# Kernel optimization log

Measured on AMD Instinct MI355X. Metric: run time of the kernel, lower is better.

The kernel has to match this reference:

```python
import jax, jax.numpy as jnp
import numpy as np

NUM_EXPERTS = 8
TOP_K = 2
HIDDEN = 2048
INTER = 7168
B, S = 4, 2048


def setup_inputs() -> dict:
    key = jax.random.key(0)
    k0, k1, k2, k3, k4 = jax.random.split(key, 5)
    scale_h = 1.0 / np.sqrt(HIDDEN)
    scale_i = 1.0 / np.sqrt(INTER)
    return {
        "hidden_states": jax.random.normal(k0, (B, S, HIDDEN), dtype=jnp.float32),
        "gate_w": jax.random.normal(k1, (NUM_EXPERTS, HIDDEN), dtype=jnp.float32) * scale_h,
        "w1": jax.random.normal(k2, (NUM_EXPERTS, INTER, HIDDEN), dtype=jnp.float32) * scale_h,
        "w3": jax.random.normal(k3, (NUM_EXPERTS, INTER, HIDDEN), dtype=jnp.float32) * scale_h,
        "w2": jax.random.normal(k4, (NUM_EXPERTS, HIDDEN, INTER), dtype=jnp.float32) * scale_i,
    }


def reference(hidden_states, gate_w, w1, w3, w2):
    orig_shape = hidden_states.shape
    x = hidden_states.reshape(-1, HIDDEN)              # [T, H]

    # Router: gate linear -> softmax -> top-k -> renormalize.
    router_logits = x @ gate_w.T                       # [T, E]
    probs = jax.nn.softmax(router_logits, axis=-1)
    topk_w, topk_idx = jax.lax.top_k(probs, TOP_K)     # [T, K]
    topk_w = topk_w / jnp.sum(topk_w, axis=-1, keepdims=True)

    # Dense combine weights: [T, E] with top-k renormalized weights scattered.
    combine = jnp.sum(
        jax.nn.one_hot(topk_idx, NUM_EXPERTS, dtype=x.dtype) * topk_w[..., None],
        axis=1,
    )                                                   # [T, E]

    out = jnp.zeros_like(x)
    # Fixed small loop over experts (structurally distinct weight matrices);
    # avoids materializing a [T, E, I] intermediate.
    for e in range(NUM_EXPERTS):
        g = jax.nn.silu(x @ w1[e].T)                   # [T, I]
        u = x @ w3[e].T                                # [T, I]
        y = (g * u) @ w2[e].T                          # [T, H]
        out = out + combine[:, e:e + 1] * y

    return out.reshape(orig_shape)
```

## Files before the change

### kernel.cpp

```cpp
#include <hip/hip_runtime.h>
#include <stdint.h>

#define NE    8
#define HID   2048
#define INTER 7168
#define TTOK  8192

typedef __bf16 bf16;
typedef bf16 bf16x4 __attribute__((ext_vector_type(4)));
typedef bf16 bf16x8 __attribute__((ext_vector_type(8)));
typedef float f32x4 __attribute__((ext_vector_type(4)));

__device__ __forceinline__ void glds16(const void* g, void* l) {
  __builtin_amdgcn_global_load_lds((__attribute__((address_space(1))) void*)g,
                                   (__attribute__((address_space(3))) void*)l, 16, 0, 0);
}

__global__ void cvt_f32_bf16(const float* __restrict__ src, bf16* __restrict__ dst, long n) {
  long i = (long)blockIdx.x * blockDim.x + threadIdx.x;
  long stride = (long)gridDim.x * blockDim.x;
  for (long j = i * 4; j < n; j += stride * 4) {
    float4 v = *(const float4*)(src + j);
    bf16x4 o = {(bf16)v.x, (bf16)v.y, (bf16)v.z, (bf16)v.w};
    *(bf16x4*)(dst + j) = o;
  }
}

__global__ void router_kernel(const float* __restrict__ x, const float* __restrict__ gw,
                              int* __restrict__ topk_e, float* __restrict__ topk_w) {
  const int wid = threadIdx.x >> 6, lane = threadIdx.x & 63;
  const int t = blockIdx.x * 4 + wid;
  if (t >= TTOK) return;
  const float* xr = x + (size_t)t * HID;
  float xv[32];
#pragma unroll
  for (int i = 0; i < 32; ++i) xv[i] = xr[lane + 64 * i];
  float lg[NE];
#pragma unroll
  for (int e = 0; e < NE; ++e) {
    const float* g = gw + e * HID;
    float s = 0.f;
#pragma unroll
    for (int i = 0; i < 32; ++i) s += xv[i] * g[lane + 64 * i];
#pragma unroll
    for (int off = 32; off; off >>= 1) s += __shfl_down(s, off);
    lg[e] = s;
  }
  if (lane == 0) {
    int i1 = 0;
#pragma unroll
    for (int e = 1; e < NE; ++e) if (lg[e] > lg[i1]) i1 = e;
    int i2 = (i1 == 0) ? 1 : 0;
#pragma unroll
    for (int e = 0; e < NE; ++e) if (e != i2 && e != i1 && lg[e] > lg[i2]) i2 = e;
    float r = __expf(lg[i2] - lg[i1]);
    float wa = 1.f / (1.f + r);
    topk_e[2 * t] = i1; topk_e[2 * t + 1] = i2;
    topk_w[2 * t] = wa; topk_w[2 * t + 1] = 1.f - wa;
  }
}

__global__ void gather_kernel(const int* __restrict__ topk_e, const float* __restrict__ topk_w,
                              int* __restrict__ cnt, int* __restrict__ ltok, float* __restrict__ lw) {
  const int t = blockIdx.x * blockDim.x + threadIdx.x;
  if (t >= TTOK) return;
#pragma unroll
  for (int j = 0; j < 2; ++j) {
    int e = topk_e[2 * t + j];
    int s = atomicAdd(&cnt[e], 1);
    ltok[e * TTOK + s] = t;
    lw[e * TTOK + s] = topk_w[2 * t + j];
  }
}

__global__ void prefix_kernel(const int* __restrict__ cnt, int* __restrict__ base) {
  if (threadIdx.x == 0 && blockIdx.x == 0) {
    int b = 0;
    for (int e = 0; e < NE; ++e) { base[e] = b; b += cnt[e]; }
  }
}

__launch_bounds__(256, 2)
__global__ void pass1_kernel(const bf16* __restrict__ xb, const bf16* __restrict__ w1b,
                             const bf16* __restrict__ w3b, bf16* __restrict__ hbuf,
                             const int* __restrict__ cnt, const int* __restrict__ base,
                             const int* __restrict__ ltok) {
  const int e = blockIdx.z;
  const int c = cnt[e];
  const int tm = blockIdx.y;
  if (tm * 128 >= c) return;
  const int tn = blockIdx.x;
  __shared__ __align__(16) bf16 lA[128 * 32];
  __shared__ __align__(16) bf16 lB1[128 * 32];
  __shared__ __align__(16) bf16 lB3[128 * 32];
  const int tid = threadIdx.x;
  const int r0 = tid >> 2, r1 = r0 + 64;
  const int sub = (tid & 3) * 16;
  int s0 = tm * 128 + r0; if (s0 >= c) s0 = c - 1;
  int s1 = tm * 128 + r1; if (s1 >= c) s1 = c - 1;
  const char* gA0 = (const char*)(xb + (size_t)ltok[e * TTOK + s0] * HID) + sub;
  const char* gA1 = (const char*)(xb + (size_t)ltok[e * TTOK + s1] * HID) + sub;
  const char* gB1r0 = (const char*)(w1b + ((size_t)e * INTER + tn * 128 + r0) * HID) + sub;
  const char* gB1r1 = (const char*)(w1b + ((size_t)e * INTER + tn * 128 + r1) * HID) + sub;
  const char* gB3r0 = (const char*)(w3b + ((size_t)e * INTER + tn * 128 + r0) * HID) + sub;
  const char* gB3r1 = (const char*)(w3b + ((size_t)e * INTER + tn * 128 + r1) * HID) + sub;
  bf16* lA0 = &lA[tid * 8];  bf16* lA1 = &lA[(tid + 256) * 8];
  bf16* lB1p0 = &lB1[tid * 8]; bf16* lB1p1 = &lB1[(tid + 256) * 8];
  bf16* lB3p0 = &lB3[tid * 8]; bf16* lB3p1 = &lB3[(tid + 256) * 8];

  const int lane = tid & 63;
  const int wid = tid >> 6;
  const int wm = wid >> 1, wn = wid & 1;
  const int ln15 = lane & 15, kq = lane >> 4;

  f32x4 ag[4][4], au[4][4];
#pragma unroll
  for (int m = 0; m < 4; ++m)
#pragma unroll
    for (int n = 0; n < 4; ++n) {
      ag[m][n] = (f32x4){0.f, 0.f, 0.f, 0.f};
      au[m][n] = (f32x4){0.f, 0.f, 0.f, 0.f};
    }

  for (int kt = 0; kt < HID / 32; ++kt) {
    const int kb = kt * 64;
    __syncthreads();
    glds16(gA0 + kb, lA0);   glds16(gA1 + kb, lA1);
    glds16(gB1r0 + kb, lB1p0); glds16(gB1r1 + kb, lB1p1);
    glds16(gB3r0 + kb, lB3p0); glds16(gB3r1 + kb, lB3p1);
    __syncthreads();
    bf16x8 af[4];
#pragma unroll
    for (int m = 0; m < 4; ++m)
      af[m] = *(const bf16x8*)&lA[(wm * 64 + m * 16 + ln15) * 32 + kq * 8];
#pragma unroll
    for (int n = 0; n < 4; ++n) {
      bf16x8 b1 = *(const bf16x8*)&lB1[(wn * 64 + n * 16 + ln15) * 32 + kq * 8];
      bf16x8 b3 = *(const bf16x8*)&lB3[(wn * 64 + n * 16 + ln15) * 32 + kq * 8];
#pragma unroll
      for (int m = 0; m < 4; ++m) {
        ag[m][n] = __builtin_amdgcn_mfma_f32_16x16x32_bf16(af[m], b1, ag[m][n], 0, 0, 0);
        au[m][n] = __builtin_amdgcn_mfma_f32_16x16x32_bf16(af[m], b3, au[m][n], 0, 0, 0);
      }
    }
  }

  const int be = base[e];
#pragma unroll
  for (int m = 0; m < 4; ++m) {
#pragma unroll
    for (int j = 0; j < 4; ++j) {
      const int slot = tm * 128 + wm * 64 + m * 16 + kq * 4 + j;
      if (slot < c) {
        bf16* hrow = hbuf + (size_t)(be + slot) * INTER + tn * 128;
#pragma unroll
        for (int n = 0; n < 4; ++n) {
          const int col = wn * 64 + n * 16 + ln15;
          const float g = ag[m][n][j];
          const float u = au[m][n][j];
          const float hv = g / (1.f + __expf(-g)) * u;
          hrow[col] = (bf16)hv;
        }
      }
    }
  }
}

__launch_bounds__(256, 2)
__global__ void pass2_kernel(const bf16* __restrict__ hbuf, const bf16* __restrict__ w2b,
                             float* __restrict__ out, const int* __restrict__ cnt,
                             const int* __restrict__ base, const int* __restrict__ ltok,
                             const float* __restrict__ lw) {
  const int e = blockIdx.z;
  const int c = cnt[e];
  const int tm = blockIdx.y;
  if (tm * 128 >= c) return;
  const int tn = blockIdx.x;
  __shared__ __align__(16) bf16 lA[128 * 32];
  __shared__ __align__(16) bf16 lB[128 * 32];
  const int tid = threadIdx.x;
  const int r0 = tid >> 2, r1 = r0 + 64;
  const int sub = (tid & 3) * 16;
  const int be = base[e];
  int s0 = tm * 128 + r0; if (s0 >= c) s0 = c - 1;
  int s1 = tm * 128 + r1; if (s1 >= c) s1 = c - 1;
  const char* gA0 = (const char*)(hbuf + (size_t)(be + s0) * INTER) + sub;
  const char* gA1 = (const char*)(hbuf + (size_t)(be + s1) * INTER) + sub;
  const char* gB0 = (const char*)(w2b + ((size_t)e * HID + tn * 128 + r0) * INTER) + sub;
  const char* gB1 = (const char*)(w2b + ((size_t)e * HID + tn * 128 + r1) * INTER) + sub;
  bf16* lA0 = &lA[tid * 8]; bf16* lA1 = &lA[(tid + 256) * 8];
  bf16* lB0 = &lB[tid * 8]; bf16* lB1p = &lB[(tid + 256) * 8];

  const int lane = tid & 63;
  const int wid = tid >> 6;
  const int wm = wid >> 1, wn = wid & 1;
  const int ln15 = lane & 15, kq = lane >> 4;

  f32x4 acc[4][4];
#pragma unroll
  for (int m = 0; m < 4; ++m)
#pragma unroll
    for (int n = 0; n < 4; ++n) acc[m][n] = (f32x4){0.f, 0.f, 0.f, 0.f};

  for (int kt = 0; kt < INTER / 32; ++kt) {
    const int kb = kt * 64;
    __syncthreads();
    glds16(gA0 + kb, lA0); glds16(gA1 + kb, lA1);
    glds16(gB0 + kb, lB0); glds16(gB1 + kb, lB1p);
    __syncthreads();
    bf16x8 af[4];
#pragma unroll
    for (int m = 0; m < 4; ++m)
      af[m] = *(const bf16x8*)&lA[(wm * 64 + m * 16 + ln15) * 32 + kq * 8];
#pragma unroll
    for (int n = 0; n < 4; ++n) {
      bf16x8 bf_ = *(const bf16x8*)&lB[(wn * 64 + n * 16 + ln15) * 32 + kq * 8];
#pragma unroll
      for (int m = 0; m < 4; ++m)
        acc[m][n] = __builtin_amdgcn_mfma_f32_16x16x32_bf16(af[m], bf_, acc[m][n], 0, 0, 0);
    }
  }

#pragma unroll
  for (int m = 0; m < 4; ++m) {
#pragma unroll
    for (int j = 0; j < 4; ++j) {
      const int slot = tm * 128 + wm * 64 + m * 16 + kq * 4 + j;
      if (slot < c) {
        const int t = ltok[e * TTOK + slot];
        const float wt = lw[e * TTOK + slot];
        float* orow = out + (size_t)t * HID + tn * 128;
#pragma unroll
        for (int n = 0; n < 4; ++n) {
          const int col = wn * 64 + n * 16 + ln15;
          atomicAdd(orow + col, wt * acc[m][n][j]);
        }
      }
    }
  }
}

extern "C" void kernel_launch(void* const* d_in, const int* in_sizes, int n_in,
                              void* d_out, int out_size, void* d_ws, size_t ws_size,
                              hipStream_t stream) {
  const float* x  = (const float*)d_in[0];
  const float* gw = (const float*)d_in[1];
  const float* w1 = (const float*)d_in[2];
  const float* w3 = (const float*)d_in[3];
  const float* w2 = (const float*)d_in[4];
  float* out = (float*)d_out;

  char* ws = (char*)d_ws;
  size_t off = 0;
  auto take = [&](size_t bytes) -> char* {
    char* p = ws + off;
    off += (bytes + 255) & ~(size_t)255;
    return p;
  };
  bf16* xb    = (bf16*)take((size_t)TTOK * HID * 2);
  bf16* w1b   = (bf16*)take((size_t)NE * INTER * HID * 2);
  bf16* w3b   = (bf16*)take((size_t)NE * INTER * HID * 2);
  bf16* w2b   = (bf16*)take((size_t)NE * HID * INTER * 2);
  bf16* hbuf  = (bf16*)take((size_t)TTOK * 2 * INTER * 2);
  int*   topk_e = (int*)take(TTOK * 2 * 4);
  float* topk_w = (float*)take(TTOK * 2 * 4);
  int*   ltok   = (int*)take(NE * TTOK * 4);
  float* lwgt   = (float*)take(NE * TTOK * 4);
  int*   cntp   = (int*)take(64);
  int*   basep  = (int*)take(64);
  if (off > ws_size) return;

  hipMemsetAsync(d_out, 0, (size_t)out_size * 4, stream);
  hipMemsetAsync(cntp, 0, 64, stream);

  cvt_f32_bf16<<<2048, 256, 0, stream>>>(x,  xb,  (long)TTOK * HID);
  cvt_f32_bf16<<<4096, 256, 0, stream>>>(w1, w1b, (long)NE * INTER * HID);
  cvt_f32_bf16<<<4096, 256, 0, stream>>>(w3, w3b, (long)NE * INTER * HID);
  cvt_f32_bf16<<<4096, 256, 0, stream>>>(w2, w2b, (long)NE * HID * INTER);

  router_kernel<<<TTOK / 4, 256, 0, stream>>>(x, gw, topk_e, topk_w);
  gather_kernel<<<TTOK / 256, 256, 0, stream>>>(topk_e, topk_w, cntp, ltok, lwgt);
  prefix_kernel<<<1, 64, 0, stream>>>(cntp, basep);

  pass1_kernel<<<dim3(INTER / 128, TTOK / 128, NE), 256, 0, stream>>>(
      xb, w1b, w3b, hbuf, cntp, basep, ltok);
  pass2_kernel<<<dim3(HID / 128, TTOK / 128, NE), 256, 0, stream>>>(
      hbuf, w2b, out, cntp, basep, ltok, lwgt);
}
```

Before: 2.324 ms.

## Rewrite expert GEMMs with 256x256 tiles, double-buffered LDS pipeline and swizzle

Both expert GEMM passes now use 512-thread blocks with 256-row token tiles and double-buffered 64-wide K stages. Global-to-LDS loads for later stages are interleaved with four MFMA phases using explicit waitcnt, barriers and setprio. LDS rows are XOR-swizzled to avoid bank conflicts. Pass1 stacks interleaved w1/w3 rows into one B tile by assuming w3b follows w1b contiguously in the workspace. The larger tiles raise data reuse and hide load latency, but increase LDS and register pressure and reduce the number of blocks.

```diff
diff --git a/kernel.cpp b/kernel.cpp
--- a/kernel.cpp
+++ b/kernel.cpp
@@ -5,6 +5,8 @@
 #define HID   2048
 #define INTER 7168
 #define TTOK  8192
+#define NT1   (HID / 64)
+#define NT2   (INTER / 64)
 
 typedef __bf16 bf16;
 typedef bf16 bf16x4 __attribute__((ext_vector_type(4)));
@@ -80,164 +82,298 @@
   }
 }
 
-__launch_bounds__(256, 2)
+
+#define MFMA(a, b, c) __builtin_amdgcn_mfma_f32_16x16x32_bf16((a), (b), (c), 0, 0, 0)
+
+#define STAGE_A(h, kt) do { int _b = ((kt) & 1) * 32768; size_t _k = (size_t)(kt) * 128; \
+    glds16(bA + oA[(h)*2 + 0] + _k, ldsA + _b + (h) * 16384 + d0); \
+    glds16(bA + oA[(h)*2 + 1] + _k, ldsA + _b + (h) * 16384 + d1); } while (0)
+#define STAGE_B(h, kt) do { int _b = ((kt) & 1) * 32768; size_t _k = (size_t)(kt) * 128; \
+    glds16(bB + oB[(h)*2 + 0] + _k, ldsB + _b + (h) * 16384 + d0); \
+    glds16(bB + oB[(h)*2 + 1] + _k, ldsB + _b + (h) * 16384 + d1); } while (0)
+
+#define RD_A(mf, ks) (*(const bf16x8*)(ldsA + curb + arow + (mf) * (16 * 128) + ((ks) ? kcol1 : kcol0)))
+#define RD_B(nf, ks) (*(const bf16x8*)(ldsB + curb + brow + (nf) * (16 * 128) + ((ks) ? kcol1 : kcol0)))
+
+#define BAR()   __builtin_amdgcn_s_barrier()
+#define LGKM0() do { asm volatile("s_waitcnt lgkmcnt(0)" ::: "memory"); \
+                     __builtin_amdgcn_sched_barrier(0); } while (0)
+
+__launch_bounds__(512, 2)
 __global__ void pass1_kernel(const bf16* __restrict__ xb, const bf16* __restrict__ w1b,
-                             const bf16* __restrict__ w3b, bf16* __restrict__ hbuf,
-                             const int* __restrict__ cnt, const int* __restrict__ base,
-                             const int* __restrict__ ltok) {
+                             bf16* __restrict__ hbuf, const int* __restrict__ cnt,
+                             const int* __restrict__ basep, const int* __restrict__ ltok) {
   const int e = blockIdx.z;
   const int c = cnt[e];
   const int tm = blockIdx.y;
-  if (tm * 128 >= c) return;
+  if (tm * 256 >= c) return;
   const int tn = blockIdx.x;
-  __shared__ __align__(16) bf16 lA[128 * 32];
-  __shared__ __align__(16) bf16 lB1[128 * 32];
-  __shared__ __align__(16) bf16 lB3[128 * 32];
+
+  __shared__ __align__(16) bf16 sA[2][256 * 64];
+  __shared__ __align__(16) bf16 sB[2][256 * 64];
+  char* const ldsA = (char*)&sA[0][0];
+  char* const ldsB = (char*)&sB[0][0];
+
   const int tid = threadIdx.x;
-  const int r0 = tid >> 2, r1 = r0 + 64;
-  const int sub = (tid & 3) * 16;
-  int s0 = tm * 128 + r0; if (s0 >= c) s0 = c - 1;
-  int s1 = tm * 128 + r1; if (s1 >= c) s1 = c - 1;
-  const char* gA0 = (const char*)(xb + (size_t)ltok[e * TTOK + s0] * HID) + sub;
-  const char* gA1 = (const char*)(xb + (size_t)ltok[e * TTOK + s1] * HID) + sub;
-  const char* gB1r0 = (const char*)(w1b + ((size_t)e * INTER + tn * 128 + r0) * HID) + sub;
-  const char* gB1r1 = (const char*)(w1b + ((size_t)e * INTER + tn * 128 + r1) * HID) + sub;
-  const char* gB3r0 = (const char*)(w3b + ((size_t)e * INTER + tn * 128 + r0) * HID) + sub;
-  const char* gB3r1 = (const char*)(w3b + ((size_t)e * INTER + tn * 128 + r1) * HID) + sub;
-  bf16* lA0 = &lA[tid * 8];  bf16* lA1 = &lA[(tid + 256) * 8];
-  bf16* lB1p0 = &lB1[tid * 8]; bf16* lB1p1 = &lB1[(tid + 256) * 8];
-  bf16* lB3p0 = &lB3[tid * 8]; bf16* lB3p1 = &lB3[(tid + 256) * 8];
-
-  const int lane = tid & 63;
-  const int wid = tid >> 6;
-  const int wm = wid >> 1, wn = wid & 1;
+  const int r0 = tid >> 3;
+  const int ls = (tid & 7) ^ (r0 & 7);
+  const int d0 = tid * 16, d1 = (tid + 512) * 16;
+  const char* const bA = (const char*)xb;
+  const char* const bB = (const char*)w1b;
+
+  uint32_t oA[4], oB[4];
+#pragma unroll
+  for (int i = 0; i < 4; ++i) {
+    int trow = i * 64 + r0;
+    int slot = tm * 256 + trow; if (slot >= c) slot = c - 1;
+    oA[i] = (uint32_t)((size_t)ltok[e * TTOK + slot] * (HID * 2) + ls * 16);
+    int br = i * 64 + r0;
+    int w = (br >> 4) & 1;
+    int wr = tn * 128 + ((br >> 5) << 4) + (br & 15);
+    size_t off = ((size_t)e * INTER + wr) * (HID * 2) + (size_t)ls * 16;
+    if (w) off += (size_t)NE * INTER * HID * 2;
+    oB[i] = (uint32_t)off;
+  }
+
+  const int lane = tid & 63, wid = tid >> 6;
+  const int wm = wid >> 2, wn = wid & 3;
   const int ln15 = lane & 15, kq = lane >> 4;
-
-  f32x4 ag[4][4], au[4][4];
-#pragma unroll
-  for (int m = 0; m < 4; ++m)
-#pragma unroll
-    for (int n = 0; n < 4; ++n) {
-      ag[m][n] = (f32x4){0.f, 0.f, 0.f, 0.f};
-      au[m][n] = (f32x4){0.f, 0.f, 0.f, 0.f};
-    }
-
-  for (int kt = 0; kt < HID / 32; ++kt) {
-    const int kb = kt * 64;
-    __syncthreads();
-    glds16(gA0 + kb, lA0);   glds16(gA1 + kb, lA1);
-    glds16(gB1r0 + kb, lB1p0); glds16(gB1r1 + kb, lB1p1);
-    glds16(gB3r0 + kb, lB3p0); glds16(gB3r1 + kb, lB3p1);
-    __syncthreads();
-    bf16x8 af[4];
-#pragma unroll
-    for (int m = 0; m < 4; ++m)
-      af[m] = *(const bf16x8*)&lA[(wm * 64 + m * 16 + ln15) * 32 + kq * 8];
-#pragma unroll
-    for (int n = 0; n < 4; ++n) {
-      bf16x8 b1 = *(const bf16x8*)&lB1[(wn * 64 + n * 16 + ln15) * 32 + kq * 8];
-      bf16x8 b3 = *(const bf16x8*)&lB3[(wn * 64 + n * 16 + ln15) * 32 + kq * 8];
-#pragma unroll
-      for (int m = 0; m < 4; ++m) {
-        ag[m][n] = __builtin_amdgcn_mfma_f32_16x16x32_bf16(af[m], b1, ag[m][n], 0, 0, 0);
-        au[m][n] = __builtin_amdgcn_mfma_f32_16x16x32_bf16(af[m], b3, au[m][n], 0, 0, 0);
-      }
-    }
-  }
-
-  const int be = base[e];
-#pragma unroll
-  for (int m = 0; m < 4; ++m) {
-#pragma unroll
-    for (int j = 0; j < 4; ++j) {
-      const int slot = tm * 128 + wm * 64 + m * 16 + kq * 4 + j;
-      if (slot < c) {
-        bf16* hrow = hbuf + (size_t)(be + slot) * INTER + tn * 128;
-#pragma unroll
-        for (int n = 0; n < 4; ++n) {
-          const int col = wn * 64 + n * 16 + ln15;
-          const float g = ag[m][n][j];
-          const float u = au[m][n][j];
-          const float hv = g / (1.f + __expf(-g)) * u;
-          hrow[col] = (bf16)hv;
+  const int swz = (ln15 & 7) << 4;
+  const int kcol0 = (kq * 16) ^ swz;
+  const int kcol1 = (64 + kq * 16) ^ swz;
+  const int arow = (wm * 128 + ln15) * 128;
+  const int brow = (wn * 64 + ln15) * 128;
+
+  f32x4 acc[8][4];
+#pragma unroll
+  for (int m = 0; m < 8; ++m)
+#pragma unroll
+    for (int n = 0; n < 4; ++n) acc[m][n] = (f32x4){0.f, 0.f, 0.f, 0.f};
+
+  STAGE_A(0, 0); STAGE_A(1, 0); STAGE_B(0, 0); STAGE_B(1, 0);
+  asm volatile("s_waitcnt vmcnt(4)" ::: "memory");
+  STAGE_A(0, 1); STAGE_A(1, 1); STAGE_B(0, 1);
+  asm volatile("s_waitcnt vmcnt(6)" ::: "memory");
+  BAR();
+
+  bf16x8 a0[4][2], a1[4][2], b0[2][2], b1[2][2];
+  int cur = 0;
+  for (int t = 0; t < NT1; ++t, cur ^= 1) {
+    const int curb = cur * 32768;
+#pragma unroll
+    for (int m = 0; m < 4; ++m) { a0[m][0] = RD_A(m, 0); a0[m][1] = RD_A(m, 1); }
+#pragma unroll
+    for (int n = 0; n < 2; ++n) { b0[n][0] = RD_B(n, 0); b0[n][1] = RD_B(n, 1); }
+    if (t + 1 < NT1) STAGE_B(1, t + 1);
+    BAR(); LGKM0();
+    __builtin_amdgcn_s_setprio(1);
+#pragma unroll
+    for (int m = 0; m < 4; ++m)
+#pragma unroll
+      for (int n = 0; n < 2; ++n) {
+        acc[m][n] = MFMA(a0[m][0], b0[n][0], acc[m][n]);
+        acc[m][n] = MFMA(a0[m][1], b0[n][1], acc[m][n]);
+      }
+    __builtin_amdgcn_s_setprio(0);
+    BAR();
+#pragma unroll
+    for (int m = 0; m < 4; ++m) { a1[m][0] = RD_A(4 + m, 0); a1[m][1] = RD_A(4 + m, 1); }
+    if (t + 2 < NT1) STAGE_A(0, t + 2);
+    BAR(); LGKM0();
+    __builtin_amdgcn_s_setprio(1);
+#pragma unroll
+    for (int m = 0; m < 4; ++m)
+#pragma unroll
+      for (int n = 0; n < 2; ++n) {
+        acc[4 + m][n] = MFMA(a1[m][0], b0[n][0], acc[4 + m][n]);
+        acc[4 + m][n] = MFMA(a1[m][1], b0[n][1], acc[4 + m][n]);
+      }
+    __builtin_amdgcn_s_setprio(0);
+    BAR();
+#pragma unroll
+    for (int n = 0; n < 2; ++n) { b1[n][0] = RD_B(2 + n, 0); b1[n][1] = RD_B(2 + n, 1); }
+    if (t + 2 < NT1) STAGE_A(1, t + 2);
+    BAR(); LGKM0();
+    __builtin_amdgcn_s_setprio(1);
+#pragma unroll
+    for (int m = 0; m < 4; ++m)
+#pragma unroll
+      for (int n = 0; n < 2; ++n) {
+        acc[m][2 + n] = MFMA(a0[m][0], b1[n][0], acc[m][2 + n]);
+        acc[m][2 + n] = MFMA(a0[m][1], b1[n][1], acc[m][2 + n]);
+      }
+    __builtin_amdgcn_s_setprio(0);
+    BAR();
+    if (t + 2 < NT1) STAGE_B(0, t + 2);
+    __builtin_amdgcn_s_setprio(1);
+#pragma unroll
+    for (int m = 0; m < 4; ++m)
+#pragma unroll
+      for (int n = 0; n < 2; ++n) {
+        acc[4 + m][2 + n] = MFMA(a1[m][0], b1[n][0], acc[4 + m][2 + n]);
+        acc[4 + m][2 + n] = MFMA(a1[m][1], b1[n][1], acc[4 + m][2 + n]);
+      }
+    __builtin_amdgcn_s_setprio(0);
+    if (t + 2 < NT1) asm volatile("s_waitcnt vmcnt(6)" ::: "memory");
+    else             asm volatile("s_waitcnt vmcnt(0)" ::: "memory");
+    BAR();
+  }
+
+  const int be = basep[e];
+#pragma unroll
+  for (int mh = 0; mh < 2; ++mh)
+#pragma unroll
+    for (int mf = 0; mf < 4; ++mf)
+#pragma unroll
+      for (int j = 0; j < 4; ++j) {
+        const int slot = tm * 256 + wm * 128 + mh * 64 + mf * 16 + kq * 4 + j;
+        if (slot < c) {
+          bf16* hrow = hbuf + (size_t)(be + slot) * INTER + tn * 128;
+#pragma unroll
+          for (int p = 0; p < 2; ++p) {
+            const float g = acc[mh * 4 + mf][2 * p][j];
+            const float u = acc[mh * 4 + mf][2 * p + 1][j];
+            const float hv = g / (1.f + __expf(-g)) * u;
+            hrow[wn * 32 + p * 16 + ln15] = (bf16)hv;
+          }
         }
       }
-    }
-  }
-}
-
-__launch_bounds__(256, 2)
+}
+
+__launch_bounds__(512, 2)
 __global__ void pass2_kernel(const bf16* __restrict__ hbuf, const bf16* __restrict__ w2b,
                              float* __restrict__ out, const int* __restrict__ cnt,
-                             const int* __restrict__ base, const int* __restrict__ ltok,
+                             const int* __restrict__ basep, const int* __restrict__ ltok,
                              const float* __restrict__ lw) {
   const int e = blockIdx.z;
   const int c = cnt[e];
   const int tm = blockIdx.y;
-  if (tm * 128 >= c) return;
+  if (tm * 256 >= c) return;
   const int tn = blockIdx.x;
-  __shared__ __align__(16) bf16 lA[128 * 32];
-  __shared__ __align__(16) bf16 lB[128 * 32];
+
+  __shared__ __align__(16) bf16 sA[2][256 * 64];
+  __shared__ __align__(16) bf16 sB[2][256 * 64];
+  char* const ldsA = (char*)&sA[0][0];
+  char* const ldsB = (char*)&sB[0][0];
+
   const int tid = threadIdx.x;
-  const int r0 = tid >> 2, r1 = r0 + 64;
-  const int sub = (tid & 3) * 16;
-  const int be = base[e];
-  int s0 = tm * 128 + r0; if (s0 >= c) s0 = c - 1;
-  int s1 = tm * 128 + r1; if (s1 >= c) s1 = c - 1;
-  const char* gA0 = (const char*)(hbuf + (size_t)(be + s0) * INTER) + sub;
-  const char* gA1 = (const char*)(hbuf + (size_t)(be + s1) * INTER) + sub;
-  const char* gB0 = (const char*)(w2b + ((size_t)e * HID + tn * 128 + r0) * INTER) + sub;
-  const char* gB1 = (const char*)(w2b + ((size_t)e * HID + tn * 128 + r1) * INTER) + sub;
-  bf16* lA0 = &lA[tid * 8]; bf16* lA1 = &lA[(tid + 256) * 8];
-  bf16* lB0 = &lB[tid * 8]; bf16* lB1p = &lB[(tid + 256) * 8];
-
-  const int lane = tid & 63;
-  const int wid = tid >> 6;
-  const int wm = wid >> 1, wn = wid & 1;
+  const int r0 = tid >> 3;
+  const int ls = (tid & 7) ^ (r0 & 7);
+  const int d0 = tid * 16, d1 = (tid + 512) * 16;
+  const int be = basep[e];
+  const char* const bA = (const char*)hbuf;
+  const char* const bB = (const char*)w2b;
+
+  uint32_t oA[4], oB[4];
+#pragma unroll
+  for (int i = 0; i < 4; ++i) {
+    int trow = i * 64 + r0;
+    int slot = tm * 256 + trow; if (slot >= c) slot = c - 1;
+    oA[i] = (uint32_t)((size_t)(be + slot) * (INTER * 2) + ls * 16);
+    int br = i * 64 + r0;
+    oB[i] = (uint32_t)(((size_t)e * HID + tn * 256 + br) * (INTER * 2) + (size_t)ls * 16);
+  }
+
+  const int lane = tid & 63, wid = tid >> 6;
+  const int wm = wid >> 2, wn = wid & 3;
   const int ln15 = lane & 15, kq = lane >> 4;
-
-  f32x4 acc[4][4];
-#pragma unroll
-  for (int m = 0; m < 4; ++m)
+  const int swz = (ln15 & 7) << 4;
+  const int kcol0 = (kq * 16) ^ swz;
+  const int kcol1 = (64 + kq * 16) ^ swz;
+  const int arow = (wm * 128 + ln15) * 128;
+  const int brow = (wn * 64 + ln15) * 128;
+
+  f32x4 acc[8][4];
+#pragma unroll
+  for (int m = 0; m < 8; ++m)
 #pragma unroll
     for (int n = 0; n < 4; ++n) acc[m][n] = (f32x4){0.f, 0.f, 0.f, 0.f};
 
-  for (int kt = 0; kt < INTER / 32; ++kt) {
-    const int kb = kt * 64;
-    __syncthreads();
-    glds16(gA0 + kb, lA0); glds16(gA1 + kb, lA1);
-    glds16(gB0 + kb, lB0); glds16(gB1 + kb, lB1p);
-    __syncthreads();
-    bf16x8 af[4];
-#pragma unroll
-    for (int m = 0; m < 4; ++m)
-      af[m] = *(const bf16x8*)&lA[(wm * 64 + m * 16 + ln15) * 32 + kq * 8];
-#pragma unroll
-    for (int n = 0; n < 4; ++n) {
-      bf16x8 bf_ = *(const bf16x8*)&lB[(wn * 64 + n * 16 + ln15) * 32 + kq * 8];
-#pragma unroll
-      for (int m = 0; m < 4; ++m)
-        acc[m][n] = __builtin_amdgcn_mfma_f32_16x16x32_bf16(af[m], bf_, acc[m][n], 0, 0, 0);
-    }
-  }
-
-#pragma unroll
-  for (int m = 0; m < 4; ++m) {
-#pragma unroll
-    for (int j = 0; j < 4; ++j) {
-      const int slot = tm * 128 + wm * 64 + m * 16 + kq * 4 + j;
-      if (slot < c) {
-        const int t = ltok[e * TTOK + slot];
-        const float wt = lw[e * TTOK + slot];
-        float* orow = out + (size_t)t * HID + tn * 128;
-#pragma unroll
-        for (int n = 0; n < 4; ++n) {
-          const int col = wn * 64 + n * 16 + ln15;
-          atomicAdd(orow + col, wt * acc[m][n][j]);
+  STAGE_A(0, 0); STAGE_A(1, 0); STAGE_B(0, 0); STAGE_B(1, 0);
+  asm volatile("s_waitcnt vmcnt(4)" ::: "memory");
+  STAGE_A(0, 1); STAGE_A(1, 1); STAGE_B(0, 1);
+  asm volatile("s_waitcnt vmcnt(6)" ::: "memory");
+  BAR();
+
+  bf16x8 a0[4][2], a1[4][2], b0[2][2], b1[2][2];
+  int cur = 0;
+  for (int t = 0; t < NT2; ++t, cur ^= 1) {
+    const int curb = cur * 32768;
+#pragma unroll
+    for (int m = 0; m < 4; ++m) { a0[m][0] = RD_A(m, 0); a0[m][1] = RD_A(m, 1); }
+#pragma unroll
+    for (int n = 0; n < 2; ++n) { b0[n][0] = RD_B(n, 0); b0[n][1] = RD_B(n, 1); }
+    if (t + 1 < NT2) STAGE_B(1, t + 1);
+    BAR(); LGKM0();
+    __builtin_amdgcn_s_setprio(1);
+#pragma unroll
+    for (int m = 0; m < 4; ++m)
+#pragma unroll
+      for (int n = 0; n < 2; ++n) {
+        acc[m][n] = MFMA(a0[m][0], b0[n][0], acc[m][n]);
+        acc[m][n] = MFMA(a0[m][1], b0[n][1], acc[m][n]);
+      }
+    __builtin_amdgcn_s_setprio(0);
+    BAR();
+#pragma unroll
+    for (int m = 0; m < 4; ++m) { a1[m][0] = RD_A(4 + m, 0); a1[m][1] = RD_A(4 + m, 1); }
+    if (t + 2 < NT2) STAGE_A(0, t + 2);
+    BAR(); LGKM0();
+    __builtin_amdgcn_s_setprio(1);
+#pragma unroll
+    for (int m = 0; m < 4; ++m)
+#pragma unroll
+      for (int n = 0; n < 2; ++n) {
+        acc[4 + m][n] = MFMA(a1[m][0], b0[n][0], acc[4 + m][n]);
+        acc[4 + m][n] = MFMA(a1[m][1], b0[n][1], acc[4 + m][n]);
+      }
+    __builtin_amdgcn_s_setprio(0);
+    BAR();
+#pragma unroll
+    for (int n = 0; n < 2; ++n) { b1[n][0] = RD_B(2 + n, 0); b1[n][1] = RD_B(2 + n, 1); }
+    if (t + 2 < NT2) STAGE_A(1, t + 2);
+    BAR(); LGKM0();
+    __builtin_amdgcn_s_setprio(1);
+#pragma unroll
+    for (int m = 0; m < 4; ++m)
+#pragma unroll
+      for (int n = 0; n < 2; ++n) {
+        acc[m][2 + n] = MFMA(a0[m][0], b1[n][0], acc[m][2 + n]);
+        acc[m][2 + n] = MFMA(a0[m][1], b1[n][1], acc[m][2 + n]);
+      }
+    __builtin_amdgcn_s_setprio(0);
+    BAR();
+    if (t + 2 < NT2) STAGE_B(0, t + 2);
+    __builtin_amdgcn_s_setprio(1);
+#pragma unroll
+    for (int m = 0; m < 4; ++m)
+#pragma unroll
+      for (int n = 0; n < 2; ++n) {
+        acc[4 + m][2 + n] = MFMA(a1[m][0], b1[n][0], acc[4 + m][2 + n]);
+        acc[4 + m][2 + n] = MFMA(a1[m][1], b1[n][1], acc[4 + m][2 + n]);
+      }
+    __builtin_amdgcn_s_setprio(0);
+    if (t + 2 < NT2) asm volatile("s_waitcnt vmcnt(6)" ::: "memory");
+    else             asm volatile("s_waitcnt vmcnt(0)" ::: "memory");
+    BAR();
+  }
+
+#pragma unroll
+  for (int mh = 0; mh < 2; ++mh)
+#pragma unroll
+    for (int mf = 0; mf < 4; ++mf)
+#pragma unroll
+      for (int j = 0; j < 4; ++j) {
+        const int slot = tm * 256 + wm * 128 + mh * 64 + mf * 16 + kq * 4 + j;
+        if (slot < c) {
+          const int tok = ltok[e * TTOK + slot];
+          const float wt = lw[e * TTOK + slot];
+          float* orow = out + (size_t)tok * HID + tn * 256;
+#pragma unroll
+          for (int n = 0; n < 4; ++n)
+            atomicAdd(orow + wn * 64 + n * 16 + ln15, wt * acc[mh * 4 + mf][n][j]);
         }
       }
-    }
-  }
 }
 
 extern "C" void kernel_launch(void* const* d_in, const int* in_sizes, int n_in,
@@ -282,8 +418,8 @@
   gather_kernel<<<TTOK / 256, 256, 0, stream>>>(topk_e, topk_w, cntp, ltok, lwgt);
   prefix_kernel<<<1, 64, 0, stream>>>(cntp, basep);
 
-  pass1_kernel<<<dim3(INTER / 128, TTOK / 128, NE), 256, 0, stream>>>(
-      xb, w1b, w3b, hbuf, cntp, basep, ltok);
-  pass2_kernel<<<dim3(HID / 128, TTOK / 128, NE), 256, 0, stream>>>(
+  pass1_kernel<<<dim3(INTER / 128, TTOK / 256, NE), 512, 0, stream>>>(
+      xb, w1b, hbuf, cntp, basep, ltok);
+  pass2_kernel<<<dim3(HID / 256, TTOK / 256, NE), 512, 0, stream>>>(
       hbuf, w2b, out, cntp, basep, ltok, lwgt);
 }
```

Result: no change. 2.292 ms (-1.4%).
